# Optimization experiments

Measured on AMD Instinct MI355X. Metric: run time of the kernel, lower is better.

Reference implementation:

```python
import jax, jax.numpy as jnp
import numpy as np

LN_EPS = 1e-5

def setup_inputs() -> dict:
    key = jax.random.key(0)
    ks = jax.random.split(key, 4)
    B, T, D = 8, 2048, 1024
    x = jax.random.normal(ks[0], (B, T, D), dtype=jnp.float32)
    Wz = jax.random.normal(ks[1], (D, D), dtype=jnp.float32) * (1.0 / np.sqrt(D))
    bz = jnp.zeros((D,), dtype=jnp.float32)
    Wh = jax.random.normal(ks[2], (D, D), dtype=jnp.float32) * (1.0 / np.sqrt(D))
    bh = jnp.zeros((D,), dtype=jnp.float32)
    swish_beta = jnp.float32(1.0)
    ln_gamma = jnp.ones((D,), dtype=jnp.float32)
    ln_beta = jnp.zeros((D,), dtype=jnp.float32)
    return {"x": x, "Wz": Wz, "bz": bz, "Wh": Wh, "bh": bh,
            "swish_beta": swish_beta, "ln_gamma": ln_gamma, "ln_beta": ln_beta}

def _min_gru(x, Wz, bz, Wh, bh):
    # x: [B,T,D]. minGRU: h_t = (1-z_t)*h_{t-1} + z_t*h_tilde_t, h_0 = 0.
    z = jax.nn.sigmoid(jnp.einsum('btd,de->bte', x, Wz) + bz)   # [B,T,D]
    h_tilde = jnp.einsum('btd,de->bte', x, Wh) + bh             # [B,T,D]
    a = 1.0 - z
    b = z * h_tilde
    # parallel associative scan over time for h_t = a_t*h_{t-1} + b_t
    def combine(c1, c2):
        a1, b1 = c1
        a2, b2 = c2
        return a1 * a2, a2 * b1 + b2
    _, h = jax.lax.associative_scan(combine, (a, b), axis=1)
    return h  # [B,T,D]

def reference(x, Wz, bz, Wh, bh, swish_beta, ln_gamma, ln_beta):
    h = _min_gru(x, Wz, bz, Wh, bh)
    # Swish with learnable beta: silu(beta*x) = (beta*x)*sigmoid(beta*x)
    s = swish_beta * h
    y = s * jax.nn.sigmoid(s)
    # LayerNorm over last dim (channels_last)
    mu = jnp.mean(y, axis=-1, keepdims=True)
    var = jnp.mean(jnp.square(y - mu), axis=-1, keepdims=True)
    out = (y - mu) * jax.lax.rsqrt(var + LN_EPS) * ln_gamma + ln_beta
    return out
```

## Files before the change

### kernel.cpp

```cpp
#include <hip/hip_runtime.h>

#define GLOBAL_AS __attribute__((address_space(1)))
#define LDS_AS __attribute__((address_space(3)))

typedef unsigned short u16;
typedef unsigned int u32;
typedef __bf16 bf16x8 __attribute__((ext_vector_type(8)));
typedef float f32x4 __attribute__((ext_vector_type(4)));

static constexpr int BB = 8;
static constexpr int TT = 2048;
static constexpr int DD = 1024;
static constexpr int MM = BB * TT;
static constexpr int KK = DD;
static constexpr int NC = 128;
static constexpr int CL = TT / NC;
static constexpr int NCH = BB * NC;

__device__ __forceinline__ u16 f2bf(float f) {
  union { float f; u32 u; } c; c.f = f;
  u32 u = c.u;
  u32 r = (u + 0x7fffu + ((u >> 16) & 1u)) >> 16;
  return (u16)r;
}

__device__ __forceinline__ float bf2f(u16 b) {
  union { u32 u; float f; } c; c.u = ((u32)b) << 16;
  return c.f;
}

__global__ void cvt_x_kernel(const float* __restrict__ x, u16* __restrict__ xb) {
  int i = (blockIdx.x * blockDim.x + threadIdx.x) * 8;
  const float4* p = reinterpret_cast<const float4*>(x + i);
  float4 v0 = p[0], v1 = p[1];
  uint4 o;
  o.x = (u32)f2bf(v0.x) | ((u32)f2bf(v0.y) << 16);
  o.y = (u32)f2bf(v0.z) | ((u32)f2bf(v0.w) << 16);
  o.z = (u32)f2bf(v1.x) | ((u32)f2bf(v1.y) << 16);
  o.w = (u32)f2bf(v1.z) | ((u32)f2bf(v1.w) << 16);
  *reinterpret_cast<uint4*>(xb + i) = o;
}

__global__ void cvt_w_kernel(const float* __restrict__ Wz, const float* __restrict__ Wh,
                             u16* __restrict__ WT) {
  __shared__ float tile[32][33];
  int w = blockIdx.z;
  const float* W = w ? Wh : Wz;
  u16* O = WT + (size_t)w * DD * KK;
  int k0 = blockIdx.y * 32;
  int n0 = blockIdx.x * 32;
  int tx = threadIdx.x, ty = threadIdx.y;
  for (int i = 0; i < 32; i += 8)
    tile[ty + i][tx] = W[(size_t)(k0 + ty + i) * DD + n0 + tx];
  __syncthreads();
  for (int i = 0; i < 32; i += 8)
    O[(size_t)(n0 + ty + i) * KK + k0 + tx] = f2bf(tile[tx][ty + i]);
}

__global__ __launch_bounds__(256, 2) void gemm_dual_kernel(
    const u16* __restrict__ xb,
    const u16* __restrict__ WT,
    const float* __restrict__ bz, const float* __restrict__ bh,
    u32* __restrict__ ab_out,
    float* __restrict__ Asum, float* __restrict__ Bsum) {
  __shared__ __align__(16) u16 As[128 * 64];
  __shared__ __align__(16) u16 Bzs[128 * 64];
  __shared__ __align__(16) u16 Bhs[128 * 64];

  int bid = blockIdx.x;
  int swz = ((bid & 7) << 7) | (bid >> 3);
  int mt = swz >> 3;
  int nt = swz & 7;
  int m0 = mt * 128, n0 = nt * 128;

  int tid = threadIdx.x;
  int lane = tid & 63;
  int wave = tid >> 6;
  int wr = wave >> 1;
  int wc = wave & 1;

  int r0 = tid >> 3;
  int cswz = ((tid & 7) ^ ((tid >> 3) & 7)) << 3;
  const u16* Ag  = xb + (size_t)(m0 + r0) * KK + cswz;
  const u16* Bzg = WT + (size_t)(n0 + r0) * KK + cswz;
  const u16* Bhg = Bzg + (size_t)DD * KK;

  u16* AsW  = As  + wave * 512;
  u16* BzsW = Bzs + wave * 512;
  u16* BhsW = Bhs + wave * 512;

  f32x4 accz[4][4];
  f32x4 acch[4][4];
#pragma unroll
  for (int i = 0; i < 4; i++)
#pragma unroll
    for (int j = 0; j < 4; j++) {
      accz[i][j] = (f32x4){0.f, 0.f, 0.f, 0.f};
      acch[i][j] = (f32x4){0.f, 0.f, 0.f, 0.f};
    }

  int fr = lane & 15;
  int fk = (lane >> 4) * 8;
  const int swx = (fr & 7) << 3;

  for (int k0i = 0; k0i < KK; k0i += 64) {
#pragma unroll
    for (int q = 0; q < 4; q++) {
      __builtin_amdgcn_global_load_lds((const GLOBAL_AS void*)(Ag  + k0i + (size_t)(q * 32) * KK),
                                       (LDS_AS void*)(AsW + q * 2048), 16, 0, 0);
      __builtin_amdgcn_global_load_lds((const GLOBAL_AS void*)(Bzg + k0i + (size_t)(q * 32) * KK),
                                       (LDS_AS void*)(BzsW + q * 2048), 16, 0, 0);
      __builtin_amdgcn_global_load_lds((const GLOBAL_AS void*)(Bhg + k0i + (size_t)(q * 32) * KK),
                                       (LDS_AS void*)(BhsW + q * 2048), 16, 0, 0);
    }
    __syncthreads();

#pragma unroll
    for (int kk = 0; kk < 64; kk += 32) {
      bf16x8 af[4], bzf[4], bhf[4];
#pragma unroll
      for (int i = 0; i < 4; i++)
        af[i] = *reinterpret_cast<const bf16x8*>(
            As + (wr * 64 + i * 16 + fr) * 64 + ((kk + fk) ^ swx));
#pragma unroll
      for (int j = 0; j < 4; j++) {
        int br = wc * 64 + j * 16 + fr;
        bzf[j] = *reinterpret_cast<const bf16x8*>(Bzs + br * 64 + ((kk + fk) ^ swx));
        bhf[j] = *reinterpret_cast<const bf16x8*>(Bhs + br * 64 + ((kk + fk) ^ swx));
      }
#pragma unroll
      for (int i = 0; i < 4; i++)
#pragma unroll
        for (int j = 0; j < 4; j++) {
          accz[i][j] = __builtin_amdgcn_mfma_f32_16x16x32_bf16(af[i], bzf[j], accz[i][j], 0, 0, 0);
          acch[i][j] = __builtin_amdgcn_mfma_f32_16x16x32_bf16(af[i], bhf[j], acch[i][j], 0, 0, 0);
        }
    }
    __syncthreads();
  }

  int quad = lane >> 4;
#pragma unroll
  for (int j = 0; j < 4; j++) {
    int n = n0 + wc * 64 + j * 16 + fr;
    float bzv = bz[n], bhv = bh[n];
#pragma unroll
    for (int i = 0; i < 4; i++) {
      float Aloc = 1.f, Bloc = 0.f;
      int mbase = m0 + wr * 64 + i * 16 + quad * 4;
#pragma unroll
      for (int r = 0; r < 4; r++) {
        float zp = accz[i][j][r] + bzv;
        float hp = acch[i][j][r] + bhv;
        float zs = 1.0f / (1.0f + __expf(-zp));
        float av = 1.0f - zs;
        float bv = zs * hp;
        u32 aq = (u32)(av * 65535.0f + 0.5f);
        if (aq > 65535u) aq = 65535u;
        u16 bb16 = f2bf(bv);
        size_t idx = (size_t)(mbase + r) * DD + n;
        ab_out[idx] = aq | ((u32)bb16 << 16);
        float avr = (float)aq * (1.0f / 65535.0f);
        float bvr = bf2f(bb16);
        Bloc = avr * Bloc + bvr;
        Aloc = avr * Aloc;
      }
      float Ao = __shfl_xor(Aloc, 16, 64);
      float Bo = __shfl_xor(Bloc, 16, 64);
      float Bc = (quad & 1) ? (Aloc * Bo + Bloc) : (Ao * Bloc + Bo);
      float Ac = Aloc * Ao;
      float Ao2 = __shfl_xor(Ac, 32, 64);
      float Bo2 = __shfl_xor(Bc, 32, 64);
      float Bck = (quad & 2) ? (Ac * Bo2 + Bc) : (Ao2 * Bc + Bo2);
      float Ack = Ac * Ao2;
      if (quad == 0) {
        int cg = mt * 8 + wr * 4 + i;
        Asum[(size_t)cg * DD + n] = Ack;
        Bsum[(size_t)cg * DD + n] = Bck;
      }
    }
  }
}

__global__ __launch_bounds__(64) void chunk_scan_kernel(
    const float* __restrict__ Asum, const float* __restrict__ Bsum,
    float* __restrict__ hin) {
  int tid = blockIdx.x * 64 + threadIdx.x;
  int d4 = (tid & 255) * 4;
  int b = tid >> 8;
  float4 h = {0.f, 0.f, 0.f, 0.f};
#pragma unroll 4
  for (int c = 0; c < NC; c++) {
    size_t i = ((size_t)(b * NC + c)) * DD + d4;
    *reinterpret_cast<float4*>(hin + i) = h;
    float4 av = *reinterpret_cast<const float4*>(Asum + i);
    float4 bv = *reinterpret_cast<const float4*>(Bsum + i);
    h.x = av.x * h.x + bv.x;
    h.y = av.y * h.y + bv.y;
    h.z = av.z * h.z + bv.z;
    h.w = av.w * h.w + bv.w;
  }
}

__global__ __launch_bounds__(256) void apply_ln_kernel(
    const u32* __restrict__ ab, const float* __restrict__ hin,
    const float* __restrict__ sbeta, const float* __restrict__ gamma,
    const float* __restrict__ lbeta, float* __restrict__ out) {
  __shared__ float ps[2][4];
  __shared__ float pq[2][4];
  int ch = blockIdx.x;
  int wv = threadIdx.x >> 6;
  int lane = threadIdx.x & 63;
  int d = wv * 256 + lane * 4;
  int b = ch >> 7, c = ch & (NC - 1);
  float sb = sbeta[0];

  float4 g4 = *reinterpret_cast<const float4*>(gamma + d);
  float4 be4 = *reinterpret_cast<const float4*>(lbeta + d);
  float4 h4 = *reinterpret_cast<const float4*>(hin + (size_t)ch * DD + d);

  size_t base = ((size_t)b * TT + (size_t)c * CL) * DD + d;

  uint4 zR[3];
#pragma unroll
  for (int p = 0; p < 3; p++)
    zR[p] = *reinterpret_cast<const uint4*>(ab + base + (size_t)p * DD);

#pragma unroll
  for (int t = 0; t < CL; t++) {
    const int slot = t % 3;
    const int pslot = t & 1;
    uint4 pv = zR[slot];
    if (t + 3 < CL)
      zR[slot] = *reinterpret_cast<const uint4*>(ab + base + (size_t)(t + 3) * DD);
    {
      union { u32 u; float f; } cb;
      const float as = 1.0f / 65535.0f;
      float av;
      av = (float)(pv.x & 0xffffu) * as; cb.u = pv.x & 0xffff0000u;
      h4.x = av * h4.x + cb.f;
      av = (float)(pv.y & 0xffffu) * as; cb.u = pv.y & 0xffff0000u;
      h4.y = av * h4.y + cb.f;
      av = (float)(pv.z & 0xffffu) * as; cb.u = pv.z & 0xffff0000u;
      h4.z = av * h4.z + cb.f;
      av = (float)(pv.w & 0xffffu) * as; cb.u = pv.w & 0xffff0000u;
      h4.w = av * h4.w + cb.f;
    }
    float sx = sb * h4.x, sy = sb * h4.y, sz = sb * h4.z, sw = sb * h4.w;
    float4 y;
    y.x = sx / (1.0f + __expf(-sx));
    y.y = sy / (1.0f + __expf(-sy));
    y.z = sz / (1.0f + __expf(-sz));
    y.w = sw / (1.0f + __expf(-sw));
    float sum = y.x + y.y + y.z + y.w;
    float sq = y.x * y.x + y.y * y.y + y.z * y.z + y.w * y.w;
#pragma unroll
    for (int o = 32; o > 0; o >>= 1) {
      sum += __shfl_xor(sum, o, 64);
      sq += __shfl_xor(sq, o, 64);
    }
    if (lane == 0) { ps[pslot][wv] = sum; pq[pslot][wv] = sq; }
    __syncthreads();
    float tot = ps[pslot][0] + ps[pslot][1] + ps[pslot][2] + ps[pslot][3];
    float totq = pq[pslot][0] + pq[pslot][1] + pq[pslot][2] + pq[pslot][3];
    float mu = tot * (1.0f / DD);
    float var = totq * (1.0f / DD) - mu * mu;
    float inv = rsqrtf(fmaxf(var, 0.f) + 1e-5f);
    float4 o4;
    o4.x = (y.x - mu) * inv * g4.x + be4.x;
    o4.y = (y.y - mu) * inv * g4.y + be4.y;
    o4.z = (y.z - mu) * inv * g4.z + be4.z;
    o4.w = (y.w - mu) * inv * g4.w + be4.w;
    *reinterpret_cast<float4*>(out + base + (size_t)t * DD) = o4;
  }
}

extern "C" void kernel_launch(void* const* d_in, const int* in_sizes, int n_in,
                              void* d_out, int out_size, void* d_ws, size_t ws_size,
                              hipStream_t stream) {
  const float* x     = (const float*)d_in[0];
  const float* Wz    = (const float*)d_in[1];
  const float* bz    = (const float*)d_in[2];
  const float* Wh    = (const float*)d_in[3];
  const float* bh    = (const float*)d_in[4];
  const float* sbeta = (const float*)d_in[5];
  const float* gamma = (const float*)d_in[6];
  const float* lbeta = (const float*)d_in[7];
  float* out = (float*)d_out;

  char* ws = (char*)d_ws;
  u16* xb     = (u16*)ws;
  u16* WT     = (u16*)(ws + 33554432);
  float* Asum = (float*)(ws + 37748736);
  float* Bsum = (float*)(ws + 41943040);
  float* hin  = (float*)(ws + 33554432);
  u32* ab     = (u32*)out;

  cvt_x_kernel<<<8192, 256, 0, stream>>>(x, xb);
  dim3 tw(32, 8), gw(32, 32, 2);
  cvt_w_kernel<<<gw, tw, 0, stream>>>(Wz, Wh, WT);
  gemm_dual_kernel<<<1024, 256, 0, stream>>>(xb, WT, bz, bh, ab, Asum, Bsum);
  chunk_scan_kernel<<<32, 64, 0, stream>>>(Asum, Bsum, hin);
  apply_ln_kernel<<<NCH, 256, 0, stream>>>(ab, hin, sbeta, gamma, lbeta, out);
}
```

Baseline: 235.3 us.

## Store within-chunk prefix (P,L) in GEMM epilogue and parallelize apply over rows

The GEMM epilogue now finishes the full within-chunk scan through wave shuffles. For each timestep it stores the cumulative decay product P and the local prefix L, quantized as u16 and bf16, in place of the per-step a and b. With that, h_t = P*h_in + L can be evaluated independently for every row. The apply/LayerNorm kernel drops its serial loop over 16 timesteps with a block-wide __syncthreads per step. Each wave now handles 4 rows, covering all 1024 channels per lane, and reduces with wave shuffles only. The risk is quantization error in the cumulative P and L and higher register pressure.

```diff
diff --git a/kernel.cpp b/kernel.cpp
--- a/kernel.cpp
+++ b/kernel.cpp
@@ -61,7 +61,7 @@
     const u16* __restrict__ xb,
     const u16* __restrict__ WT,
     const float* __restrict__ bz, const float* __restrict__ bh,
-    u32* __restrict__ ab_out,
+    u32* __restrict__ pl_out,
     float* __restrict__ Asum, float* __restrict__ Bsum) {
   __shared__ __align__(16) u16 As[128 * 64];
   __shared__ __align__(16) u16 Bzs[128 * 64];
@@ -146,8 +146,8 @@
     float bzv = bz[n], bhv = bh[n];
 #pragma unroll
     for (int i = 0; i < 4; i++) {
+      float pA[4], pB[4];
       float Aloc = 1.f, Bloc = 0.f;
-      int mbase = m0 + wr * 64 + i * 16 + quad * 4;
 #pragma unroll
       for (int r = 0; r < 4; r++) {
         float zp = accz[i][j][r] + bzv;
@@ -155,15 +155,9 @@
         float zs = 1.0f / (1.0f + __expf(-zp));
         float av = 1.0f - zs;
         float bv = zs * hp;
-        u32 aq = (u32)(av * 65535.0f + 0.5f);
-        if (aq > 65535u) aq = 65535u;
-        u16 bb16 = f2bf(bv);
-        size_t idx = (size_t)(mbase + r) * DD + n;
-        ab_out[idx] = aq | ((u32)bb16 << 16);
-        float avr = (float)aq * (1.0f / 65535.0f);
-        float bvr = bf2f(bb16);
-        Bloc = avr * Bloc + bvr;
-        Aloc = avr * Aloc;
+        Bloc = av * Bloc + bv;
+        Aloc = av * Aloc;
+        pA[r] = Aloc; pB[r] = Bloc;
       }
       float Ao = __shfl_xor(Aloc, 16, 64);
       float Bo = __shfl_xor(Bloc, 16, 64);
@@ -173,6 +167,18 @@
       float Bo2 = __shfl_xor(Bc, 32, 64);
       float Bck = (quad & 2) ? (Ac * Bo2 + Bc) : (Ao2 * Bc + Bo2);
       float Ack = Ac * Ao2;
+      float Ae = (quad == 0) ? 1.f : (quad == 1) ? Ao : (quad == 2) ? Ao2 : (Ao * Ao2);
+      float Be = (quad == 0) ? 0.f : (quad == 1) ? Bo : (quad == 2) ? Bo2 : (Ao * Bo2 + Bo);
+      int mbase = m0 + wr * 64 + i * 16 + quad * 4;
+#pragma unroll
+      for (int r = 0; r < 4; r++) {
+        float Pf = pA[r] * Ae;
+        float Lf = pA[r] * Be + pB[r];
+        u32 pq_ = (u32)(Pf * 65535.0f + 0.5f);
+        if (pq_ > 65535u) pq_ = 65535u;
+        u16 lb = f2bf(Lf);
+        pl_out[(size_t)(mbase + r) * DD + n] = pq_ | ((u32)lb << 16);
+      }
       if (quad == 0) {
         int cg = mt * 8 + wr * 4 + i;
         Asum[(size_t)cg * DD + n] = Ack;
@@ -203,75 +209,78 @@
 }
 
 __global__ __launch_bounds__(256) void apply_ln_kernel(
-    const u32* __restrict__ ab, const float* __restrict__ hin,
+    const u32* __restrict__ pl, const float* __restrict__ hin,
     const float* __restrict__ sbeta, const float* __restrict__ gamma,
     const float* __restrict__ lbeta, float* __restrict__ out) {
-  __shared__ float ps[2][4];
-  __shared__ float pq[2][4];
   int ch = blockIdx.x;
   int wv = threadIdx.x >> 6;
   int lane = threadIdx.x & 63;
-  int d = wv * 256 + lane * 4;
+  int d0 = lane * 4;
   int b = ch >> 7, c = ch & (NC - 1);
   float sb = sbeta[0];
 
-  float4 g4 = *reinterpret_cast<const float4*>(gamma + d);
-  float4 be4 = *reinterpret_cast<const float4*>(lbeta + d);
-  float4 h4 = *reinterpret_cast<const float4*>(hin + (size_t)ch * DD + d);
-
-  size_t base = ((size_t)b * TT + (size_t)c * CL) * DD + d;
-
-  uint4 zR[3];
-#pragma unroll
-  for (int p = 0; p < 3; p++)
-    zR[p] = *reinterpret_cast<const uint4*>(ab + base + (size_t)p * DD);
-
-#pragma unroll
-  for (int t = 0; t < CL; t++) {
-    const int slot = t % 3;
-    const int pslot = t & 1;
-    uint4 pv = zR[slot];
-    if (t + 3 < CL)
-      zR[slot] = *reinterpret_cast<const uint4*>(ab + base + (size_t)(t + 3) * DD);
-    {
-      union { u32 u; float f; } cb;
-      const float as = 1.0f / 65535.0f;
-      float av;
-      av = (float)(pv.x & 0xffffu) * as; cb.u = pv.x & 0xffff0000u;
-      h4.x = av * h4.x + cb.f;
-      av = (float)(pv.y & 0xffffu) * as; cb.u = pv.y & 0xffff0000u;
-      h4.y = av * h4.y + cb.f;
-      av = (float)(pv.z & 0xffffu) * as; cb.u = pv.z & 0xffff0000u;
-      h4.z = av * h4.z + cb.f;
-      av = (float)(pv.w & 0xffffu) * as; cb.u = pv.w & 0xffff0000u;
-      h4.w = av * h4.w + cb.f;
-    }
-    float sx = sb * h4.x, sy = sb * h4.y, sz = sb * h4.z, sw = sb * h4.w;
-    float4 y;
-    y.x = sx / (1.0f + __expf(-sx));
-    y.y = sy / (1.0f + __expf(-sy));
-    y.z = sz / (1.0f + __expf(-sz));
-    y.w = sw / (1.0f + __expf(-sw));
-    float sum = y.x + y.y + y.z + y.w;
-    float sq = y.x * y.x + y.y * y.y + y.z * y.z + y.w * y.w;
+  float4 g4[4], be4[4], hi4[4];
+#pragma unroll
+  for (int q = 0; q < 4; q++) {
+    g4[q]  = *reinterpret_cast<const float4*>(gamma + d0 + q * 256);
+    be4[q] = *reinterpret_cast<const float4*>(lbeta + d0 + q * 256);
+    hi4[q] = *reinterpret_cast<const float4*>(hin + (size_t)ch * DD + d0 + q * 256);
+  }
+
+  size_t rowbase = ((size_t)b * TT + (size_t)c * CL + wv * 4) * DD + d0;
+
+  uint4 pv[4];
+#pragma unroll
+  for (int q = 0; q < 4; q++)
+    pv[q] = *reinterpret_cast<const uint4*>(pl + rowbase + q * 256);
+
+#pragma unroll
+  for (int r = 0; r < 4; r++) {
+    uint4 nv[4];
+    if (r + 1 < 4) {
+#pragma unroll
+      for (int q = 0; q < 4; q++)
+        nv[q] = *reinterpret_cast<const uint4*>(pl + rowbase + (size_t)(r + 1) * DD + q * 256);
+    }
+    float4 y[4];
+    float sum = 0.f, sq = 0.f;
+    const float is = 1.0f / 65535.0f;
+#pragma unroll
+    for (int q = 0; q < 4; q++) {
+      union { u32 u; float f; } cl_;
+      float P, h, s;
+      P = (float)(pv[q].x & 0xffffu) * is; cl_.u = pv[q].x & 0xffff0000u;
+      h = P * hi4[q].x + cl_.f; s = sb * h; y[q].x = s / (1.0f + __expf(-s));
+      P = (float)(pv[q].y & 0xffffu) * is; cl_.u = pv[q].y & 0xffff0000u;
+      h = P * hi4[q].y + cl_.f; s = sb * h; y[q].y = s / (1.0f + __expf(-s));
+      P = (float)(pv[q].z & 0xffffu) * is; cl_.u = pv[q].z & 0xffff0000u;
+      h = P * hi4[q].z + cl_.f; s = sb * h; y[q].z = s / (1.0f + __expf(-s));
+      P = (float)(pv[q].w & 0xffffu) * is; cl_.u = pv[q].w & 0xffff0000u;
+      h = P * hi4[q].w + cl_.f; s = sb * h; y[q].w = s / (1.0f + __expf(-s));
+      sum += y[q].x + y[q].y + y[q].z + y[q].w;
+      sq  += y[q].x * y[q].x + y[q].y * y[q].y + y[q].z * y[q].z + y[q].w * y[q].w;
+    }
 #pragma unroll
     for (int o = 32; o > 0; o >>= 1) {
       sum += __shfl_xor(sum, o, 64);
-      sq += __shfl_xor(sq, o, 64);
-    }
-    if (lane == 0) { ps[pslot][wv] = sum; pq[pslot][wv] = sq; }
-    __syncthreads();
-    float tot = ps[pslot][0] + ps[pslot][1] + ps[pslot][2] + ps[pslot][3];
-    float totq = pq[pslot][0] + pq[pslot][1] + pq[pslot][2] + pq[pslot][3];
-    float mu = tot * (1.0f / DD);
-    float var = totq * (1.0f / DD) - mu * mu;
+      sq  += __shfl_xor(sq, o, 64);
+    }
+    float mu = sum * (1.0f / DD);
+    float var = sq * (1.0f / DD) - mu * mu;
     float inv = rsqrtf(fmaxf(var, 0.f) + 1e-5f);
-    float4 o4;
-    o4.x = (y.x - mu) * inv * g4.x + be4.x;
-    o4.y = (y.y - mu) * inv * g4.y + be4.y;
-    o4.z = (y.z - mu) * inv * g4.z + be4.z;
-    o4.w = (y.w - mu) * inv * g4.w + be4.w;
-    *reinterpret_cast<float4*>(out + base + (size_t)t * DD) = o4;
+#pragma unroll
+    for (int q = 0; q < 4; q++) {
+      float4 o4;
+      o4.x = (y[q].x - mu) * inv * g4[q].x + be4[q].x;
+      o4.y = (y[q].y - mu) * inv * g4[q].y + be4[q].y;
+      o4.z = (y[q].z - mu) * inv * g4[q].z + be4[q].z;
+      o4.w = (y[q].w - mu) * inv * g4[q].w + be4[q].w;
+      *reinterpret_cast<float4*>(out + rowbase + (size_t)r * DD + q * 256) = o4;
+    }
+    if (r + 1 < 4) {
+#pragma unroll
+      for (int q = 0; q < 4; q++) pv[q] = nv[q];
+    }
   }
 }
 
@@ -294,12 +303,12 @@
   float* Asum = (float*)(ws + 37748736);
   float* Bsum = (float*)(ws + 41943040);
   float* hin  = (float*)(ws + 33554432);
-  u32* ab     = (u32*)out;
+  u32* pl     = (u32*)out;
 
   cvt_x_kernel<<<8192, 256, 0, stream>>>(x, xb);
   dim3 tw(32, 8), gw(32, 32, 2);
   cvt_w_kernel<<<gw, tw, 0, stream>>>(Wz, Wh, WT);
-  gemm_dual_kernel<<<1024, 256, 0, stream>>>(xb, WT, bz, bh, ab, Asum, Bsum);
+  gemm_dual_kernel<<<1024, 256, 0, stream>>>(xb, WT, bz, bh, pl, Asum, Bsum);
   chunk_scan_kernel<<<32, 64, 0, stream>>>(Asum, Bsum, hin);
-  apply_ln_kernel<<<NCH, 256, 0, stream>>>(ab, hin, sbeta, gamma, lbeta, out);
-}
+  apply_ln_kernel<<<NCH, 256, 0, stream>>>(pl, hin, sbeta, gamma, lbeta, out);
+}
```

Measured after the change: 234.8 us. No clear change (-0.2%).
